# Kernel optimization log

Hardware: AMD Instinct MI355X
Metric: run time of the kernel (lower is better)

Reference implementation:

```python
import jax, jax.numpy as jnp
import numpy as np

B, T, C, H = 2, 2048, 1024, 16
D = C // H  # head_dim = 64


def setup_inputs() -> dict:
    key = jax.random.key(0)
    k1, k2, k3 = jax.random.split(key, 3)
    x = jax.random.normal(k1, (B, T, C), dtype=jnp.float32)
    Wqkv = jax.random.normal(k2, (C, 3 * C), dtype=jnp.float32) * (1.0 / np.sqrt(C))
    Wo = jax.random.normal(k3, (C, C), dtype=jnp.float32) * (1.0 / np.sqrt(C))
    bo = jnp.zeros((C,), dtype=jnp.float32)
    return {"x": x, "Wqkv": Wqkv, "Wo": Wo, "bo": bo}


def reference(x, Wqkv, Wo, bo):
    Bc, Tc, Cc = x.shape
    qkv = x @ Wqkv                                  # [B,T,3C]
    q, k, v = jnp.split(qkv, 3, axis=-1)
    # [B,T,C] -> [B,H,T,D]
    q = q.reshape(Bc, Tc, H, D).transpose(0, 2, 1, 3)
    k = k.reshape(Bc, Tc, H, D).transpose(0, 2, 1, 3)
    v = v.reshape(Bc, Tc, H, D).transpose(0, 2, 1, 3)
    scale = 1.0 / np.sqrt(D)
    att = jnp.einsum('bhqd,bhkd->bhqk', q, k) * scale   # [B,H,T,T]
    causal = jnp.tril(jnp.ones((Tc, Tc), dtype=bool))
    att = jnp.where(causal[None, None], att, -jnp.inf)
    att = jax.nn.softmax(att, axis=-1)
    # dropout treated as identity (eval mode)
    y = jnp.einsum('bhqk,bhkd->bhqd', att, v)           # [B,H,T,D]
    y = y.transpose(0, 2, 1, 3).reshape(Bc, Tc, Cc)     # [B,T,C]
    return y @ Wo + bo
```

## Files before the change

kernel.cpp:

```cpp
#include <hip/hip_runtime.h>
#include <hip/hip_bf16.h>
#include <math.h>


typedef __attribute__((ext_vector_type(8))) short bf16x8;
typedef __attribute__((ext_vector_type(4))) float f32x4;

__device__ __forceinline__ float b2f(unsigned short u) {
    union { unsigned int i; float f; } x; x.i = ((unsigned int)u) << 16; return x.f;
}
__device__ __forceinline__ unsigned short f2b(float f) {
    __hip_bfloat16 h = __float2bfloat16(f);
    return *reinterpret_cast<unsigned short*>(&h);
}
__device__ __forceinline__ unsigned short f2b_rz(float f) {
    union { float f; unsigned int i; } u; u.f = f; return (unsigned short)(u.i >> 16);
}
__device__ __forceinline__ float fexp2(float x) {
#if __has_builtin(__builtin_amdgcn_exp2f)
    return __builtin_amdgcn_exp2f(x);
#else
    return exp2f(x);
#endif
}
__device__ __forceinline__ void gload_lds16(const void* g, void* l) {
    __builtin_amdgcn_global_load_lds(
        (__attribute__((address_space(1))) void*)g,
        (__attribute__((address_space(3))) void*)l, 16, 0, 0);
}

__device__ __forceinline__ void transpose_job64(
        const void* __restrict__ in, unsigned short* __restrict__ out,
        int Cc, int use_bf, int nscale, float scale,
        int c0, int r0, int tid, unsigned short (*t)[65]) {
    const unsigned short* inb = (const unsigned short*)in;
    const float* inf = (const float*)in;
    const int xl = (tid & 15) * 4;
    const int y  = tid >> 4;
    const float sc = (c0 < nscale) ? scale : 1.0f;
    #pragma unroll
    for (int p = 0; p < 4; p++) {
        int row = y + 16 * p;
        float v0, v1, v2, v3;
        if (use_bf) {
            ushort4 u = *(const ushort4*)(inb + (size_t)(r0 + row) * Cc + c0 + xl);
            v0 = b2f(u.x); v1 = b2f(u.y); v2 = b2f(u.z); v3 = b2f(u.w);
        } else {
            float4 f = *(const float4*)(inf + (size_t)(r0 + row) * Cc + c0 + xl);
            v0 = f.x; v1 = f.y; v2 = f.z; v3 = f.w;
        }
        t[row][xl + 0] = f2b(v0 * sc);
        t[row][xl + 1] = f2b(v1 * sc);
        t[row][xl + 2] = f2b(v2 * sc);
        t[row][xl + 3] = f2b(v3 * sc);
    }
    __syncthreads();
    const int rr = (tid & 15) * 4;
    const int cc = tid >> 4;
    #pragma unroll
    for (int p = 0; p < 4; p++) {
        int ccp = cc + 16 * p;
        ushort4 o4;
        o4.x = t[rr + 0][ccp];
        o4.y = t[rr + 1][ccp];
        o4.z = t[rr + 2][ccp];
        o4.w = t[rr + 3][ccp];
        *(ushort4*)(out + (size_t)(c0 + ccp) * 1024 + r0 + rr) = o4;
    }
}

__global__ __launch_bounds__(256) void prep_kernel(
        const void* __restrict__ xin, const void* __restrict__ Wqkv,
        const void* __restrict__ Wo, const void* __restrict__ bias,
        unsigned short* __restrict__ xb, unsigned short* __restrict__ WqkvT,
        unsigned short* __restrict__ WoT, unsigned short* __restrict__ bob,
        int* __restrict__ flag, float qscale) {
    __shared__ __align__(16) unsigned short t[64][65];
    __shared__ int det;
    const int tid = threadIdx.x, blk = blockIdx.x;

    if (tid < 64) {
        const unsigned short* xu = (const unsigned short*)xin;
        int cnt = 0;
        for (int i = tid; i < 1024; i += 64) {
            unsigned short u = xu[2 * i];
            int e = (u >> 7) & 0xFF;
            if (!((e == 0) || (e >= 96 && e <= 159))) cnt++;
        }
        #pragma unroll
        for (int m = 1; m < 64; m <<= 1) cnt += __shfl_xor(cnt, m);
        if (tid == 0) det = (cnt > 200) ? 0 : 1;
    }
    __syncthreads();
    const int use_bf = det;

    if (blk < 1024) {
        int base = blk * 4096;
        #pragma unroll
        for (int i = 0; i < 4; i++) {
            int i4 = base + (tid + 256 * i) * 4;
            if (use_bf) {
                *(ushort4*)(xb + i4) = *(const ushort4*)((const unsigned short*)xin + i4);
            } else {
                float4 f = *(const float4*)((const float*)xin + i4);
                ushort4 o;
                o.x = f2b(f.x); o.y = f2b(f.y); o.z = f2b(f.z); o.w = f2b(f.w);
                *(ushort4*)(xb + i4) = o;
            }
        }
    } else if (blk < 1792) {
        int tt = blk - 1024;
        int c0 = (tt % 48) * 64, r0 = (tt / 48) * 64;
        transpose_job64(Wqkv, WqkvT, 3072, use_bf, 1024, qscale, c0, r0, tid, t);
    } else if (blk < 2048) {
        int tt = blk - 1792;
        int c0 = (tt & 15) * 64, r0 = (tt >> 4) * 64;
        transpose_job64(Wo, WoT, 1024, use_bf, 0, 1.0f, c0, r0, tid, t);
    } else {
        int i4 = tid * 4;
        if (use_bf) {
            *(ushort4*)(bob + i4) = *(const ushort4*)((const unsigned short*)bias + i4);
        } else {
            float4 f = *(const float4*)((const float*)bias + i4);
            ushort4 o;
            o.x = f2b(f.x); o.y = f2b(f.y); o.z = f2b(f.z); o.w = f2b(f.w);
            *(ushort4*)(bob + i4) = o;
        }
        if (tid == 0) *flag = use_bf;
    }
}

__global__ __launch_bounds__(256, 2) void gemm_qkv(
        const unsigned short* __restrict__ A, const unsigned short* __restrict__ Bt,
        unsigned short* __restrict__ qb, unsigned short* __restrict__ kb,
        unsigned short* __restrict__ vt) {
    __shared__ __align__(16) unsigned short lA[128 * 64];
    __shared__ __align__(16) unsigned short lB[192 * 64];
    const int tid  = threadIdx.x;
    const int wave = tid >> 6, lane = tid & 63;
    const int g = lane >> 4, c = lane & 15;
    const int m0 = blockIdx.y * 128, n0 = blockIdx.x * 192;
    const int wr = (wave >> 1) * 64;
    const int wc = (wave & 1) * 96;
    const int srow = lane >> 3;
    const int sc8  = ((lane & 7) ^ ((lane >> 3) & 7)) * 8;

    f32x4 acc[4][6] = {};

    for (int k0 = 0; k0 < 1024; k0 += 64) {
        #pragma unroll
        for (int i = 0; i < 4; i++) {
            int seg = wave * 4 + i;
            int row = seg * 8 + srow;
            gload_lds16(A  + (size_t)(m0 + row) * 1024 + k0 + sc8, lA + seg * 512);
        }
        #pragma unroll
        for (int i = 0; i < 6; i++) {
            int seg = wave * 6 + i;
            int row = seg * 8 + srow;
            gload_lds16(Bt + (size_t)(n0 + row) * 1024 + k0 + sc8, lB + seg * 512);
        }
        __syncthreads();

        #pragma unroll
        for (int dk = 0; dk < 2; dk++) {
            const int off = ((4 * dk + g) ^ (c & 7)) << 3;
            bf16x8 af[4], bfv[6];
            #pragma unroll
            for (int i = 0; i < 4; i++)
                af[i]  = *(const bf16x8*)(lA + (wr + 16 * i + c) * 64 + off);
            #pragma unroll
            for (int i = 0; i < 6; i++)
                bfv[i] = *(const bf16x8*)(lB + (wc + 16 * i + c) * 64 + off);
            #pragma unroll
            for (int mi = 0; mi < 4; mi++)
                #pragma unroll
                for (int ni = 0; ni < 6; ni++)
                    acc[mi][ni] = __builtin_amdgcn_mfma_f32_16x16x32_bf16(
                        af[mi], bfv[ni], acc[mi][ni], 0, 0, 0);
        }
        __syncthreads();
    }

    const int bb  = m0 >> 11;
    const int kvb = (m0 & 2047) + wr;
    #pragma unroll
    for (int ni = 0; ni < 6; ni++) {
        const int colbase = n0 + wc + 16 * ni;
        if (colbase < 2048) {
            unsigned short* dst = (colbase < 1024) ? qb : kb;
            const int cb = (colbase & 1023) + c;
            #pragma unroll
            for (int mi = 0; mi < 4; mi++)
                #pragma unroll
                for (int r = 0; r < 4; r++) {
                    int row = m0 + wr + 16 * mi + 4 * g + r;
                    dst[(size_t)row * 1024 + cb] = f2b(acc[mi][ni][r]);
                }
        } else {
            const int cc2 = colbase - 2048;
            const int hb  = cc2 >> 6;
            const int d   = (cc2 & 63) + c;
            const int bh  = bb * 16 + hb;
            #pragma unroll
            for (int mi = 0; mi < 4; mi++) {
                int kv = kvb + 16 * mi + 4 * g;
                ushort4 pk;
                pk.x = f2b(acc[mi][ni][0]); pk.y = f2b(acc[mi][ni][1]);
                pk.z = f2b(acc[mi][ni][2]); pk.w = f2b(acc[mi][ni][3]);
                *(ushort4*)(vt + ((size_t)bh * 64 + d) * 2048 + kv) = pk;
            }
        }
    }
}

__global__ __launch_bounds__(256) void gemm_nt(
        const unsigned short* __restrict__ A, const unsigned short* __restrict__ Bt,
        void* __restrict__ C, const unsigned short* __restrict__ bias,
        const int* __restrict__ out_f32_flag, int M, int N, int K) {
    __shared__ __align__(16) unsigned short lA[128 * 64];
    __shared__ __align__(16) unsigned short lB[64 * 64];
    const int tid  = threadIdx.x;
    const int wave = tid >> 6, lane = tid & 63;
    const int g = lane >> 4, c = lane & 15;
    const int m0 = blockIdx.y * 128, n0 = blockIdx.x * 64;
    const int wm = wave * 32;
    const int srow = lane >> 3;
    const int sc8  = ((lane & 7) ^ ((lane >> 3) & 7)) * 8;

    f32x4 acc[2][4] = {};

    for (int k0 = 0; k0 < K; k0 += 64) {
        #pragma unroll
        for (int i = 0; i < 4; i++) {
            int seg = wave * 4 + i;
            int row = seg * 8 + srow;
            gload_lds16(A + (size_t)(m0 + row) * K + k0 + sc8, lA + seg * 512);
        }
        #pragma unroll
        for (int i = 0; i < 2; i++) {
            int seg = wave * 2 + i;
            int row = seg * 8 + srow;
            gload_lds16(Bt + (size_t)(n0 + row) * K + k0 + sc8, lB + seg * 512);
        }
        __syncthreads();

        #pragma unroll
        for (int dk = 0; dk < 2; dk++) {
            const int off = ((4 * dk + g) ^ (c & 7)) << 3;
            bf16x8 af[2], bfv[4];
            #pragma unroll
            for (int i = 0; i < 2; i++)
                af[i]  = *(const bf16x8*)(lA + (wm + 16 * i + c) * 64 + off);
            #pragma unroll
            for (int i = 0; i < 4; i++)
                bfv[i] = *(const bf16x8*)(lB + (16 * i + c) * 64 + off);
            #pragma unroll
            for (int mi = 0; mi < 2; mi++)
                #pragma unroll
                for (int ni = 0; ni < 4; ni++)
                    acc[mi][ni] = __builtin_amdgcn_mfma_f32_16x16x32_bf16(
                        af[mi], bfv[ni], acc[mi][ni], 0, 0, 0);
        }
        __syncthreads();
    }

    const bool f32out = out_f32_flag && (*out_f32_flag == 0);
    #pragma unroll
    for (int mi = 0; mi < 2; mi++)
        #pragma unroll
        for (int ni = 0; ni < 4; ni++)
            #pragma unroll
            for (int r = 0; r < 4; r++) {
                int row = m0 + wm + 16 * mi + 4 * g + r;
                int col = n0 + 16 * ni + c;
                float v = acc[mi][ni][r];
                if (bias) v += b2f(bias[col]);
                if (f32out) ((float*)C)[(size_t)row * N + col] = v;
                else ((unsigned short*)C)[(size_t)row * N + col] = f2b(v);
            }
}

template<bool MASKED>
__device__ __forceinline__ void tile_compute(
        const unsigned short* __restrict__ lKs, const unsigned short* __restrict__ lVts,
        unsigned short* __restrict__ P, const bf16x8* qB, f32x4* o,
        float& l_run, int wave, int lane, int g, int c) {
    const f32x4 sinit = {-12.f, -12.f, -12.f, -12.f};
    f32x4 s[4] = {sinit, sinit, sinit, sinit};
    #pragma unroll
    for (int nt = 0; nt < 4; nt++)
        #pragma unroll
        for (int dk = 0; dk < 2; dk++) {
            bf16x8 kA = *(const bf16x8*)(lKs + (16 * nt + c) * 64 + (((4 * dk + g) ^ (c & 7)) << 3));
            s[nt] = __builtin_amdgcn_mfma_f32_16x16x32_bf16(kA, qB[dk], s[nt], 0, 0, 0);
        }

    bf16x8 vf[4][2];
    #pragma unroll
    for (int ni = 0; ni < 4; ni++)
        #pragma unroll
        for (int kk = 0; kk < 2; kk++)
            vf[ni][kk] = *(const bf16x8*)(lVts + (16 * ni + c) * 64 + (((4 * kk + g) ^ (c & 7)) << 3));

    float rsum = 0.f;
    #pragma unroll
    for (int nt = 0; nt < 4; nt++) {
        unsigned long long pk = 0;
        #pragma unroll
        for (int r = 0; r < 4; r++) {
            float v = s[nt][r];
            if (MASKED) v = (16 * nt + 4 * g + r <= 16 * wave + c) ? v : -1e30f;
            float p = fexp2(v);
            rsum += p;
            pk |= ((unsigned long long)f2b_rz(p)) << (16 * r);
        }
        int kvl = 16 * nt + 4 * g;
        *(unsigned long long*)(P + c * 64 + (((kvl >> 3) ^ (c & 7)) << 3) + (kvl & 7)) = pk;
    }
    rsum += __shfl_xor(rsum, 16);
    rsum += __shfl_xor(rsum, 32);
    l_run += rsum;

    __asm__ volatile("" ::: "memory");

    bf16x8 pf[2];
    #pragma unroll
    for (int kk = 0; kk < 2; kk++)
        pf[kk] = *(const bf16x8*)(P + c * 64 + (((4 * kk + g) ^ (c & 7)) << 3));
    #pragma unroll
    for (int ni = 0; ni < 4; ni++)
        #pragma unroll
        for (int kk = 0; kk < 2; kk++)
            o[ni] = __builtin_amdgcn_mfma_f32_16x16x32_bf16(pf[kk], vf[ni][kk], o[ni], 0, 0, 0);
    __asm__ volatile("" ::: "memory");
}

__global__ __launch_bounds__(256, 2) void attn_kernel(
        const unsigned short* __restrict__ qb, const unsigned short* __restrict__ kb,
        const unsigned short* __restrict__ vt, unsigned short* __restrict__ Y) {
    __shared__ __align__(16) unsigned short lK[2][4096];
    __shared__ __align__(16) unsigned short lVt[2][4096];
    __shared__ __align__(16) unsigned short Pbuf[4][1024];

    const int tid = threadIdx.x, wave = tid >> 6, lane = tid & 63;
    const int g = lane >> 4, c = lane & 15;
    unsigned short* P = Pbuf[wave];
    const int srow = lane >> 3;
    const int sc8  = ((lane & 7) ^ ((lane >> 3) & 7)) * 8;

    const int bh = blockIdx.x & 31;
    const int jp = blockIdx.x >> 5;
    const int b = bh >> 4, h = bh & 15;

    const unsigned short* Qb  = qb + (size_t)b * 2048 * 1024 + h * 64;
    const unsigned short* Kb  = kb + (size_t)b * 2048 * 1024 + h * 64;
    const unsigned short* Vtb = vt + (size_t)bh * 64 * 2048;

    #pragma unroll 1
    for (int item = 0; item < 2; item++) {
        const int j  = item ? (31 - jp) : jp;
        const int q0 = j * 64;
        const int rbase = q0 + 16 * wave;

        bf16x8 qB[2];
        #pragma unroll
        for (int dk = 0; dk < 2; dk++)
            qB[dk] = *(const bf16x8*)(Qb + (size_t)(rbase + c) * 1024 + 32 * dk + 8 * g);

        f32x4 o[4] = {};
        float l_run = 0.f;

        #pragma unroll 1
        for (int kv0 = 0; kv0 <= q0; kv0 += 128) {
            const bool do1 = (kv0 + 64 <= q0);
            #pragma unroll
            for (int i = 0; i < 2; i++) {
                int seg = wave * 2 + i;
                int row = seg * 8 + srow;
                gload_lds16(Kb  + (size_t)(kv0 + row) * 1024 + sc8, lK[0] + seg * 512);
                gload_lds16(Vtb + (size_t)row * 2048 + kv0 + sc8,   lVt[0] + seg * 512);
                if (do1) {
                    gload_lds16(Kb  + (size_t)(kv0 + 64 + row) * 1024 + sc8, lK[1] + seg * 512);
                    gload_lds16(Vtb + (size_t)row * 2048 + kv0 + 64 + sc8,   lVt[1] + seg * 512);
                }
            }
            __syncthreads();

            if (kv0 == q0)
                tile_compute<true >(lK[0], lVt[0], P, qB, o, l_run, wave, lane, g, c);
            else
                tile_compute<false>(lK[0], lVt[0], P, qB, o, l_run, wave, lane, g, c);
            if (do1) {
                if (kv0 + 64 == q0)
                    tile_compute<true >(lK[1], lVt[1], P, qB, o, l_run, wave, lane, g, c);
                else
                    tile_compute<false>(lK[1], lVt[1], P, qB, o, l_run, wave, lane, g, c);
            }
            __syncthreads();
        }

        float inv = 1.f / l_run;
        float il[4];
        #pragma unroll
        for (int r = 0; r < 4; r++)
            il[r] = __shfl(inv, (lane & 48) | (4 * g + r));
        #pragma unroll
        for (int ni = 0; ni < 4; ni++)
            #pragma unroll
            for (int r = 0; r < 4; r++) {
                int row = rbase + 4 * g + r;
                Y[(size_t)(b * 2048 + row) * 1024 + h * 64 + 16 * ni + c] =
                    f2b(o[ni][r] * il[r]);
            }
    }
}

extern "C" void kernel_launch(void* const* d_in, const int* in_sizes, int n_in,
                              void* d_out, int out_size, void* d_ws, size_t ws_size,
                              hipStream_t stream) {
    char* ws = (char*)d_ws;
    unsigned short* qb    = (unsigned short*)(ws);
    unsigned short* kb    = (unsigned short*)(ws + 8388608);
    unsigned short* vt    = (unsigned short*)(ws + 16777216);
    unsigned short* Y     = (unsigned short*)(ws + 25165824);
    unsigned short* WqkvT = (unsigned short*)(ws + 33554432);
    unsigned short* WoT   = (unsigned short*)(ws + 39845888);
    unsigned short* xb    = (unsigned short*)(ws + 41943040);
    unsigned short* bob   = (unsigned short*)(ws + 50331648);
    int*            flag  = (int*)(ws + 50333696);

    prep_kernel<<<2049, 256, 0, stream>>>(
        d_in[0], d_in[1], d_in[2], d_in[3], xb, WqkvT, WoT, bob, flag,
        0.125f * 1.4426950408889634f);

    gemm_qkv<<<dim3(16, 32), 256, 0, stream>>>(xb, WqkvT, qb, kb, vt);

    attn_kernel<<<512, 256, 0, stream>>>(qb, kb, vt, Y);

    gemm_nt<<<dim3(16, 32), 256, 0, stream>>>(Y, WoT, d_out, bob, flag, 4096, 1024, 1024);
}
```

Measured before the change: 170.5 us.

## Process both paired query tiles in one KV sweep to share K/V loads

Each block previously ran its two causal query tiles (j and 31-j) one after another, loading the K/V tiles for each separately. Now both query tiles are kept live and a single sweep over KV up to the later tile feeds both, so the KV prefix shared by the two tiles is loaded into LDS only once. This roughly halves the global-to-LDS traffic and barrier count per block. In exchange, each wave holds two sets of Q fragments, accumulators and row sums, which raises register pressure and may reduce occupancy.

Result: no change. 167.3 us (-1.9%).

```diff
diff --git a/kernel.cpp b/kernel.cpp
--- a/kernel.cpp
+++ b/kernel.cpp
@@ -357,63 +357,79 @@
     const unsigned short* Kb  = kb + (size_t)b * 2048 * 1024 + h * 64;
     const unsigned short* Vtb = vt + (size_t)bh * 64 * 2048;
 
+    const int q0a = jp * 64;
+    const int q0b = (31 - jp) * 64;
+    const int rba = q0a + 16 * wave;
+    const int rbb = q0b + 16 * wave;
+
+    bf16x8 qA[2], qBv[2];
+    #pragma unroll
+    for (int dk = 0; dk < 2; dk++) {
+        qA[dk]  = *(const bf16x8*)(Qb + (size_t)(rba + c) * 1024 + 32 * dk + 8 * g);
+        qBv[dk] = *(const bf16x8*)(Qb + (size_t)(rbb + c) * 1024 + 32 * dk + 8 * g);
+    }
+
+    f32x4 oa[4] = {}, ob[4] = {};
+    float la = 0.f, lb = 0.f;
+
     #pragma unroll 1
-    for (int item = 0; item < 2; item++) {
-        const int j  = item ? (31 - jp) : jp;
-        const int q0 = j * 64;
-        const int rbase = q0 + 16 * wave;
-
-        bf16x8 qB[2];
-        #pragma unroll
-        for (int dk = 0; dk < 2; dk++)
-            qB[dk] = *(const bf16x8*)(Qb + (size_t)(rbase + c) * 1024 + 32 * dk + 8 * g);
-
-        f32x4 o[4] = {};
-        float l_run = 0.f;
-
-        #pragma unroll 1
-        for (int kv0 = 0; kv0 <= q0; kv0 += 128) {
-            const bool do1 = (kv0 + 64 <= q0);
-            #pragma unroll
-            for (int i = 0; i < 2; i++) {
-                int seg = wave * 2 + i;
-                int row = seg * 8 + srow;
-                gload_lds16(Kb  + (size_t)(kv0 + row) * 1024 + sc8, lK[0] + seg * 512);
-                gload_lds16(Vtb + (size_t)row * 2048 + kv0 + sc8,   lVt[0] + seg * 512);
-                if (do1) {
-                    gload_lds16(Kb  + (size_t)(kv0 + 64 + row) * 1024 + sc8, lK[1] + seg * 512);
-                    gload_lds16(Vtb + (size_t)row * 2048 + kv0 + 64 + sc8,   lVt[1] + seg * 512);
-                }
+    for (int kv0 = 0; kv0 <= q0b; kv0 += 128) {
+        const bool do1 = (kv0 + 64 <= q0b);
+        #pragma unroll
+        for (int i = 0; i < 2; i++) {
+            int seg = wave * 2 + i;
+            int row = seg * 8 + srow;
+            gload_lds16(Kb  + (size_t)(kv0 + row) * 1024 + sc8, lK[0] + seg * 512);
+            gload_lds16(Vtb + (size_t)row * 2048 + kv0 + sc8,   lVt[0] + seg * 512);
+            if (do1) {
+                gload_lds16(Kb  + (size_t)(kv0 + 64 + row) * 1024 + sc8, lK[1] + seg * 512);
+                gload_lds16(Vtb + (size_t)row * 2048 + kv0 + 64 + sc8,   lVt[1] + seg * 512);
             }
-            __syncthreads();
-
-            if (kv0 == q0)
-                tile_compute<true >(lK[0], lVt[0], P, qB, o, l_run, wave, lane, g, c);
+        }
+        __syncthreads();
+
+        if (kv0 == q0b)
+            tile_compute<true >(lK[0], lVt[0], P, qBv, ob, lb, wave, lane, g, c);
+        else
+            tile_compute<false>(lK[0], lVt[0], P, qBv, ob, lb, wave, lane, g, c);
+        if (kv0 <= q0a) {
+            if (kv0 == q0a)
+                tile_compute<true >(lK[0], lVt[0], P, qA, oa, la, wave, lane, g, c);
             else
-                tile_compute<false>(lK[0], lVt[0], P, qB, o, l_run, wave, lane, g, c);
-            if (do1) {
-                if (kv0 + 64 == q0)
-                    tile_compute<true >(lK[1], lVt[1], P, qB, o, l_run, wave, lane, g, c);
+                tile_compute<false>(lK[0], lVt[0], P, qA, oa, la, wave, lane, g, c);
+        }
+        if (do1) {
+            const int kvt = kv0 + 64;
+            if (kvt == q0b)
+                tile_compute<true >(lK[1], lVt[1], P, qBv, ob, lb, wave, lane, g, c);
+            else
+                tile_compute<false>(lK[1], lVt[1], P, qBv, ob, lb, wave, lane, g, c);
+            if (kvt <= q0a) {
+                if (kvt == q0a)
+                    tile_compute<true >(lK[1], lVt[1], P, qA, oa, la, wave, lane, g, c);
                 else
-                    tile_compute<false>(lK[1], lVt[1], P, qB, o, l_run, wave, lane, g, c);
+                    tile_compute<false>(lK[1], lVt[1], P, qA, oa, la, wave, lane, g, c);
             }
-            __syncthreads();
-        }
-
-        float inv = 1.f / l_run;
-        float il[4];
-        #pragma unroll
-        for (int r = 0; r < 4; r++)
-            il[r] = __shfl(inv, (lane & 48) | (4 * g + r));
-        #pragma unroll
-        for (int ni = 0; ni < 4; ni++)
-            #pragma unroll
-            for (int r = 0; r < 4; r++) {
-                int row = rbase + 4 * g + r;
-                Y[(size_t)(b * 2048 + row) * 1024 + h * 64 + 16 * ni + c] =
-                    f2b(o[ni][r] * il[r]);
-            }
-    }
+        }
+        __syncthreads();
+    }
+
+    float inva = 1.f / la, invb = 1.f / lb;
+    float ila[4], ilb[4];
+    #pragma unroll
+    for (int r = 0; r < 4; r++) {
+        ila[r] = __shfl(inva, (lane & 48) | (4 * g + r));
+        ilb[r] = __shfl(invb, (lane & 48) | (4 * g + r));
+    }
+    #pragma unroll
+    for (int ni = 0; ni < 4; ni++)
+        #pragma unroll
+        for (int r = 0; r < 4; r++) {
+            Y[(size_t)(b * 2048 + rba + 4 * g + r) * 1024 + h * 64 + 16 * ni + c] =
+                f2b(oa[ni][r] * ila[r]);
+            Y[(size_t)(b * 2048 + rbb + 4 * g + r) * 1024 + h * 64 + 16 * ni + c] =
+                f2b(ob[ni][r] * ilb[r]);
+        }
 }
 
 extern "C" void kernel_launch(void* const* d_in, const int* in_sizes, int n_in,
```
